# Optimization experiments

Measured on AMD Instinct MI355X. Metric: run time of the kernel, lower is better.

Reference implementation:

```python
import jax, jax.numpy as jnp
import numpy as np

N = 50000      # num_nodes
E = 800000     # num_edges
F = 29         # num_node_features
IN = F + 3     # in_channels after hstack with pos
H = 64         # hidden_dim
B = 50         # batch_size (num graphs)
L = 7          # num GINConv layers


def setup_inputs() -> dict:
    key = jax.random.key(0)
    ks = jax.random.split(key, 12)
    s_in = 1.0 / np.sqrt(IN)
    s_h = 1.0 / np.sqrt(H)
    return {
        "x": jax.random.normal(ks[0], (N, F), jnp.float32),
        "pos": jax.random.normal(ks[1], (N, 3), jnp.float32),
        "edge_index": jax.random.randint(ks[2], (2, E), 0, N),
        "batch": jnp.sort(jax.random.randint(ks[3], (N,), 0, B)),
        # GINConv l: MLP = Linear(in,H) -> ReLU -> Linear(H,H)
        "W1_first": jax.random.normal(ks[4], (IN, H), jnp.float32) * s_in,
        "W1_rest": jax.random.normal(ks[5], (L - 1, H, H), jnp.float32) * s_h,
        "b1": jax.random.normal(ks[6], (L, H), jnp.float32) * 0.01,
        "W2": jax.random.normal(ks[7], (L, H, H), jnp.float32) * s_h,
        "b2": jax.random.normal(ks[8], (L, H), jnp.float32) * 0.01,
        "lin_w": jax.random.normal(ks[9], (H, 1), jnp.float32) * s_h,
        "lin_b": jax.random.normal(ks[10], (1,), jnp.float32) * 0.01,
    }


def reference(x, pos, edge_index, batch, W1_first, W1_rest, b1, W2, b2, lin_w, lin_b):
    src, dst = edge_index[0], edge_index[1]
    h = jnp.concatenate([x, pos], axis=1)  # [N, IN]

    def gin_conv(h, Wa, ba, Wb, bb):
        # sum aggregation of source features at destination nodes, eps=0
        agg = jax.ops.segment_sum(h[src], dst, num_segments=N)
        z = h + agg
        z = jax.nn.relu(z @ Wa + ba)
        return z @ Wb + bb

    h = jax.nn.relu(gin_conv(h, W1_first, b1[0], W2[0], b2[0]))
    for l in range(1, L):
        h = gin_conv(h, W1_rest[l - 1], b1[l], W2[l], b2[l])
        if l < L - 1:  # no activation after last conv (jk=None)
            h = jax.nn.relu(h)

    # global mean pool per graph
    sums = jax.ops.segment_sum(h, batch, num_segments=B)            # [B, H]
    counts = jax.ops.segment_sum(jnp.ones((N,), h.dtype), batch, num_segments=B)
    pooled = sums / jnp.maximum(counts, 1.0)[:, None]

    return pooled @ lin_w + lin_b  # [B, 1]
```

## Files before the change

### kernel.cpp

```cpp
#include <hip/hip_runtime.h>
#include <stdint.h>

#define NF 29
#define HD 64
#define NL 7
#define LDW 72
#define NCHUNK 256
#define BSH 8
#define PER_M (64 * LDW)

typedef __attribute__((ext_vector_type(8))) __bf16 bf16x8;
typedef __attribute__((ext_vector_type(4))) float floatx4;
typedef int int32x4 __attribute__((ext_vector_type(4)));
typedef float f32x4v __attribute__((ext_vector_type(4)));

extern "C" __device__ f32x4v llvm_amdgcn_raw_buffer_load_fp32x4(
    int32x4 srsrc, int voffset, int soffset, int cachepolicy)
    __asm("llvm.amdgcn.raw.buffer.load.v4f32");

__device__ __forceinline__ int32x4 make_srd(const void* p) {
    unsigned long long a = (unsigned long long)p;
    int32x4 r;
    r.x = (int)(a & 0xFFFFFFFFull);
    r.y = (int)(a >> 32);
    r.z = -1;
    r.w = 0x00020000;
    return r;
}
__device__ __forceinline__ uint4 bload16_sc0(int32x4 srd, int voff) {
    f32x4v v = llvm_amdgcn_raw_buffer_load_fp32x4(srd, voff, 0, 1 );
    union { f32x4v f; uint4 u; } c;
    c.f = v;
    return c.u;
}

__device__ __forceinline__ unsigned short f2bf(float x) {
    unsigned u = __float_as_uint(x);
    unsigned r = (u + 0x7fffu + ((u >> 16) & 1u)) >> 16;
    return (unsigned short)r;
}
__device__ __forceinline__ unsigned pack_bf2(float x, float y) {
    return (unsigned)f2bf(x) | ((unsigned)f2bf(y) << 16);
}
__device__ __forceinline__ float bflo(uint32_t u) { return __uint_as_float(u << 16); }
__device__ __forceinline__ float bfhi(uint32_t u) { return __uint_as_float(u & 0xffff0000u); }
__device__ __forceinline__ float bf2f(unsigned short s) {
    return __uint_as_float((uint32_t)s << 16);
}

__global__ void front_kernel(const float* __restrict__ x, const float* __restrict__ pos,
                             unsigned short* __restrict__ h0,
                             const float* __restrict__ W1f, const float* __restrict__ W1r,
                             const float* __restrict__ W2, unsigned short* __restrict__ wpk,
                             const int* __restrict__ dst, int E, int chunk,
                             int* __restrict__ bcnt, int* __restrict__ bsum,
                             float* __restrict__ pool, int N, int B) {
    __shared__ int hist[256];
    const int H0B = (N * 4 + 255) / 256;
    const int WPB = (NL * 2 * PER_M + 255) / 256;
    int blk = blockIdx.x;
    if (blk < H0B) {
        int t = blk * 256 + threadIdx.x;
        if (t < N * 4) {
            int n = t >> 2, q = t & 3;
            const float* xr = x + (size_t)n * NF;
            float f[8];
            if (q < 3) {
                #pragma unroll
                for (int i = 0; i < 8; ++i) f[i] = xr[q * 8 + i];
            } else {
                #pragma unroll
                for (int i = 0; i < 5; ++i) f[i] = xr[24 + i];
                f[5] = pos[n * 3 + 0]; f[6] = pos[n * 3 + 1]; f[7] = pos[n * 3 + 2];
            }
            uint4 pk;
            pk.x = pack_bf2(f[0], f[1]); pk.y = pack_bf2(f[2], f[3]);
            pk.z = pack_bf2(f[4], f[5]); pk.w = pack_bf2(f[6], f[7]);
            ((uint4*)h0)[t] = pk;
        }
    } else if (blk < H0B + WPB) {
        int bw = blk - H0B;
        if (bw == 0) {
            for (int i = threadIdx.x; i < B * HD; i += 256) pool[i] = 0.f;
        }
        int t = bw * 256 + threadIdx.x;
        if (t < NL * 2 * PER_M) {
            int l = t / (2 * PER_M);
            int r = t - l * 2 * PER_M;
            int m = r / PER_M;
            int q = r - m * PER_M;
            int j = q / LDW, k = q - j * LDW;
            float v = 0.f;
            if (m == 0) {
                int ind = (l == 0) ? 32 : 64;
                if (k < ind) v = (l == 0) ? W1f[k * 64 + j]
                                          : W1r[(size_t)(l - 1) * 4096 + (size_t)k * 64 + j];
            } else {
                if (k < 64) v = W2[(size_t)l * 4096 + (size_t)k * 64 + j];
            }
            wpk[t] = f2bf(v);
        }
    } else {
        int c = blk - H0B - WPB;
        int tid = threadIdx.x;
        hist[tid] = 0;
        __syncthreads();
        int lo = c * chunk, hi = min(E, lo + chunk);
        for (int e = lo + tid; e < hi; e += 256) atomicAdd(&hist[dst[e] >> BSH], 1);
        __syncthreads();
        bcnt[tid * NCHUNK + c] = hist[tid];
        if (hist[tid]) atomicAdd(&bsum[tid], hist[tid]);
    }
}

__global__ void bucket_off_kernel(const int* __restrict__ bcnt, const int* __restrict__ bsum,
                                  int* __restrict__ boffT) {
    __shared__ int red[256];
    __shared__ int s[256];
    int b = blockIdx.x, t = threadIdx.x;
    red[t] = (t < b) ? bsum[t] : 0;
    __syncthreads();
    #pragma unroll
    for (int off = 128; off > 0; off >>= 1) {
        if (t < off) red[t] += red[t + off];
        __syncthreads();
    }
    int bstart_b = red[0];
    int c = bcnt[b * NCHUNK + t];
    s[t] = c;
    __syncthreads();
    for (int off = 1; off < 256; off <<= 1) {
        int v = (t >= off) ? s[t - off] : 0;
        __syncthreads();
        s[t] += v;
        __syncthreads();
    }
    int excl = s[t] - c;
    boffT[t * 256 + b] = bstart_b + excl;
}

__global__ void bucket_scatter_kernel(const int* __restrict__ src, const int* __restrict__ dst,
                                      int E, int chunk, const int* __restrict__ boffT,
                                      unsigned int* __restrict__ ebuf) {
    __shared__ int cur[256];
    int tid = threadIdx.x, c = blockIdx.x;
    cur[tid] = boffT[c * 256 + tid];
    __syncthreads();
    int lo = c * chunk, hi = min(E, lo + chunk);
    for (int e = lo + tid; e < hi; e += 256) {
        int d = dst[e];
        int p = atomicAdd(&cur[d >> BSH], 1);
        ebuf[p] = (unsigned int)src[e] | ((unsigned int)(d & 255) << 16);
    }
}

__global__ void final_scatter_kernel(const unsigned int* __restrict__ ebuf,
                                     const int* __restrict__ bsum,
                                     int* __restrict__ rowptr,
                                     unsigned short* __restrict__ colsrc, int N, int E) {
    __shared__ int red[256];
    __shared__ int cnt[256];
    __shared__ int cur[256];
    __shared__ int s[256];
    int b = blockIdx.x, t = threadIdx.x;
    red[t] = (t < b) ? bsum[t] : 0;
    cnt[t] = 0;
    __syncthreads();
    #pragma unroll
    for (int off = 128; off > 0; off >>= 1) {
        if (t < off) red[t] += red[t + off];
        __syncthreads();
    }
    int lo = red[0];
    int hi = lo + bsum[b];
    if (b == 0 && t == 0) rowptr[N] = E;
    for (int e = lo + t; e < hi; e += 256) atomicAdd(&cnt[ebuf[e] >> 16], 1);
    __syncthreads();
    int c = cnt[t];
    s[t] = c;
    __syncthreads();
    for (int off = 1; off < 256; off <<= 1) {
        int v = (t >= off) ? s[t - off] : 0;
        __syncthreads();
        s[t] += v;
        __syncthreads();
    }
    int base = lo + s[t] - c;
    int node = (b << BSH) + t;
    if (node < N) rowptr[node] = base;
    cur[t] = base;
    __syncthreads();
    for (int e = lo + t; e < hi; e += 256) {
        unsigned int ed = ebuf[e];
        int p = atomicAdd(&cur[ed >> 16], 1);
        colsrc[p] = (unsigned short)(ed & 0xffffu);
    }
}

template<int IND, bool RELU_OUT, bool LAST>
__global__ __launch_bounds__(512, 8)
void gin_layer_kernel(const unsigned short* __restrict__ hin,
                      const int* __restrict__ rowptr, const unsigned short* __restrict__ colsrc,
                      const unsigned short* __restrict__ wAT, const unsigned short* __restrict__ wBT,
                      const float* __restrict__ ba, const float* __restrict__ bb,
                      unsigned short* __restrict__ hout,
                      const int* __restrict__ batch, float* __restrict__ pool,
                      int N)
{
    __shared__ __align__(16) unsigned short zbuf[64 * LDW];
    __shared__ __align__(16) unsigned short t1buf[64 * LDW];

    const int tid = threadIdx.x;
    const int lane = tid & 63;
    const int w = tid >> 6;
    const int tile0 = blockIdx.x * 64;

    const int32x4 srd = make_srd(hin);
    const int g = lane >> 3;
    const int j = lane & 7;
    const int node = tile0 + w * 8 + g;

    int rp;
    {
        int idx = tile0 + w * 8 + (lane < 9 ? lane : 8);
        if (idx > N) idx = N;
        rp = rowptr[idx];
    }
    int e0 = __shfl(rp, g);
    int e1 = __shfl(rp, g + 1);
    if (node >= N) { e0 = 0; e1 = 0; }

    float acc[8] = {0.f, 0.f, 0.f, 0.f, 0.f, 0.f, 0.f, 0.f};
    auto addrow = [&](uint4 u) {
        acc[0] += bflo(u.x); acc[1] += bfhi(u.x);
        acc[2] += bflo(u.y); acc[3] += bfhi(u.y);
        acc[4] += bflo(u.z); acc[5] += bfhi(u.z);
        acc[6] += bflo(u.w); acc[7] += bfhi(u.w);
    };

    if constexpr (IND == 64) {
        const int f4 = lane & 7;
        if (node < N) addrow(bload16_sc0(srd, node * 128 + f4 * 16));
        int e = e0;
        int idxv = (e + j < e1) ? (int)colsrc[e + j] : 0;
        for (; e + 7 < e1; e += 8) {
            int en = e + 8;
            int idx_next = (en + j < e1) ? (int)colsrc[en + j] : 0;
            int s[8];
            #pragma unroll
            for (int q = 0; q < 8; ++q) s[q] = __shfl(idxv, g * 8 + q);
            uint4 u[8];
            #pragma unroll
            for (int q = 0; q < 8; ++q) u[q] = bload16_sc0(srd, s[q] * 128 + f4 * 16);
            #pragma unroll
            for (int q = 0; q < 8; ++q) addrow(u[q]);
            idxv = idx_next;
        }
        {
            int rem = e1 - e;
            #pragma unroll
            for (int q = 0; q < 8; ++q) {
                if (q < rem) {
                    int s = __shfl(idxv, g * 8 + q);
                    addrow(bload16_sc0(srd, s * 128 + f4 * 16));
                }
            }
        }
        uint4 pk;
        pk.x = pack_bf2(acc[0], acc[1]); pk.y = pack_bf2(acc[2], acc[3]);
        pk.z = pack_bf2(acc[4], acc[5]); pk.w = pack_bf2(acc[6], acc[7]);
        *(uint4*)&zbuf[(w * 8 + g) * LDW + f4 * 8] = pk;
    } else {
        const int p = (lane >> 2) & 1;
        const int f4 = lane & 3;
        if (node < N && p == 0) addrow(bload16_sc0(srd, node * 64 + f4 * 16));
        int e = e0 + p;
        for (; e + 7 < e1; e += 8) {
            int s0 = colsrc[e], s1 = colsrc[e + 2], s2 = colsrc[e + 4], s3 = colsrc[e + 6];
            uint4 u0 = bload16_sc0(srd, s0 * 64 + f4 * 16);
            uint4 u1 = bload16_sc0(srd, s1 * 64 + f4 * 16);
            uint4 u2 = bload16_sc0(srd, s2 * 64 + f4 * 16);
            uint4 u3 = bload16_sc0(srd, s3 * 64 + f4 * 16);
            addrow(u0); addrow(u1); addrow(u2); addrow(u3);
        }
        while (e < e1) { addrow(bload16_sc0(srd, (int)colsrc[e] * 64 + f4 * 16)); e += 2; }
        #pragma unroll
        for (int i = 0; i < 8; ++i) acc[i] += __shfl_xor(acc[i], 4);
        if (p == 0) {
            uint4 pk;
            pk.x = pack_bf2(acc[0], acc[1]); pk.y = pack_bf2(acc[2], acc[3]);
            pk.z = pack_bf2(acc[4], acc[5]); pk.w = pack_bf2(acc[6], acc[7]);
            *(uint4*)&zbuf[(w * 8 + g) * LDW + f4 * 8] = pk;
        }
    }
    __syncthreads();

    const int n0 = lane & 15, quad = lane >> 4;
    const int stripe = w & 3, jhalf = w >> 2;
    const int row0 = stripe * 16;
    const int jt0 = jhalf * 2, jt1 = jhalf * 2 + 1;

    floatx4 c0, c1;
    {
        float b0v = ba[jt0 * 16 + n0], b1v = ba[jt1 * 16 + n0];
        c0 = (floatx4){b0v, b0v, b0v, b0v};
        c1 = (floatx4){b1v, b1v, b1v, b1v};
    }
    #pragma unroll
    for (int kk = 0; kk < IND / 32; ++kk) {
        bf16x8 a   = *(const bf16x8*)&zbuf[(row0 + n0) * LDW + kk * 32 + quad * 8];
        bf16x8 br0 = *(const bf16x8*)&wAT[(jt0 * 16 + n0) * LDW + kk * 32 + quad * 8];
        bf16x8 br1 = *(const bf16x8*)&wAT[(jt1 * 16 + n0) * LDW + kk * 32 + quad * 8];
        c0 = __builtin_amdgcn_mfma_f32_16x16x32_bf16(a, br0, c0, 0, 0, 0);
        c1 = __builtin_amdgcn_mfma_f32_16x16x32_bf16(a, br1, c1, 0, 0, 0);
    }
    #pragma unroll
    for (int r = 0; r < 4; ++r) {
        int row = row0 + quad * 4 + r;
        t1buf[row * LDW + jt0 * 16 + n0] = f2bf(fmaxf(c0[r], 0.f));
        t1buf[row * LDW + jt1 * 16 + n0] = f2bf(fmaxf(c1[r], 0.f));
    }
    __syncthreads();

    {
        float b0v = bb[jt0 * 16 + n0], b1v = bb[jt1 * 16 + n0];
        c0 = (floatx4){b0v, b0v, b0v, b0v};
        c1 = (floatx4){b1v, b1v, b1v, b1v};
    }
    #pragma unroll
    for (int kk = 0; kk < 2; ++kk) {
        bf16x8 a   = *(const bf16x8*)&t1buf[(row0 + n0) * LDW + kk * 32 + quad * 8];
        bf16x8 br0 = *(const bf16x8*)&wBT[(jt0 * 16 + n0) * LDW + kk * 32 + quad * 8];
        bf16x8 br1 = *(const bf16x8*)&wBT[(jt1 * 16 + n0) * LDW + kk * 32 + quad * 8];
        c0 = __builtin_amdgcn_mfma_f32_16x16x32_bf16(a, br0, c0, 0, 0, 0);
        c1 = __builtin_amdgcn_mfma_f32_16x16x32_bf16(a, br1, c1, 0, 0, 0);
    }
    #pragma unroll
    for (int r = 0; r < 4; ++r) {
        int row = row0 + quad * 4 + r;
        float v0 = c0[r], v1 = c1[r];
        if (RELU_OUT) { v0 = fmaxf(v0, 0.f); v1 = fmaxf(v1, 0.f); }
        zbuf[row * LDW + jt0 * 16 + n0] = f2bf(v0);
        zbuf[row * LDW + jt1 * 16 + n0] = f2bf(v1);
    }
    __syncthreads();

    if constexpr (!LAST) {
        int nl = tid >> 3, c4 = tid & 7;
        int nodeo = tile0 + nl;
        if (nodeo < N) {
            uint4 v = *(const uint4*)&zbuf[nl * LDW + c4 * 8];
            ((uint4*)hout)[(size_t)nodeo * 8 + c4] = v;
        }
    } else {
        int nl0 = w * 8;
        int bvec = 0;
        if (lane < 8) {
            int idx = tile0 + nl0 + lane;
            bvec = batch[idx < N ? idx : (N - 1)];
        }
        int bsel = -1;
        float run = 0.f;
        for (int i = 0; i < 8; ++i) {
            int nodeo = tile0 + nl0 + i;
            if (nodeo >= N) break;
            int b = __shfl(bvec, i);
            float v = bf2f(zbuf[(nl0 + i) * LDW + lane]);
            if (b != bsel) {
                if (bsel >= 0) atomicAdd(&pool[bsel * HD + lane], run);
                bsel = b; run = 0.f;
            }
            run += v;
        }
        if (bsel >= 0) atomicAdd(&pool[bsel * HD + lane], run);
    }
}

__global__ void final_kernel(const float* __restrict__ pool, const int* __restrict__ batch,
                             const float* __restrict__ lin_w, const float* __restrict__ lin_b,
                             float* __restrict__ out, int B, int N) {
    int b = blockIdx.x;
    int lane = threadIdx.x;
    int lo = 0, hi = N;
    while (lo < hi) { int m = (lo + hi) >> 1; if (batch[m] < b) lo = m + 1; else hi = m; }
    int lb = lo;
    lo = 0; hi = N;
    while (lo < hi) { int m = (lo + hi) >> 1; if (batch[m] <= b) lo = m + 1; else hi = m; }
    float c = fmaxf((float)(lo - lb), 1.f);
    float v = pool[b * HD + lane] / c * lin_w[lane];
    for (int off = 32; off > 0; off >>= 1) v += __shfl_down(v, off);
    if (lane == 0) out[b] = v + lin_b[0];
}

extern "C" void kernel_launch(void* const* d_in, const int* in_sizes, int n_in,
                              void* d_out, int out_size, void* d_ws, size_t ws_size,
                              hipStream_t stream)
{
    const float* x   = (const float*)d_in[0];
    const float* pos = (const float*)d_in[1];
    const int*  eidx = (const int*)d_in[2];
    const int* batch = (const int*)d_in[3];
    const float* W1f = (const float*)d_in[4];
    const float* W1r = (const float*)d_in[5];
    const float* b1  = (const float*)d_in[6];
    const float* W2  = (const float*)d_in[7];
    const float* b2  = (const float*)d_in[8];
    const float* lw  = (const float*)d_in[9];
    const float* lb  = (const float*)d_in[10];

    int N = in_sizes[3];
    int E = in_sizes[2] / 2;
    int B = out_size;
    const int* src = eidx;
    const int* dst = eidx + E;

    char* ws = (char*)d_ws;
    size_t off = 0;
    auto alloc = [&](size_t bytes) -> void* {
        void* p = ws + off;
        off += (bytes + 255) & ~(size_t)255;
        return p;
    };
    unsigned short* bufA = (unsigned short*)alloc((size_t)N * HD * 2);
    unsigned short* bufB = (unsigned short*)alloc((size_t)N * HD * 2);
    int*   rowptr = (int*)  alloc((size_t)(N + 1) * 4);
    unsigned short* colsrc = (unsigned short*)alloc((size_t)E * 2);
    unsigned int* ebuf = (unsigned int*)alloc((size_t)E * 4);
    float* pool   = (float*)alloc((size_t)B * HD * 4);
    int*   bcnt   = (int*)  alloc((size_t)256 * NCHUNK * 4);
    int*   boffT  = (int*)  alloc((size_t)NCHUNK * 256 * 4);
    int*   bsum   = (int*)  alloc(256 * 4);
    unsigned short* wpk = (unsigned short*)alloc((size_t)NL * 2 * PER_M * 2);

    hipMemsetAsync(bsum, 0, 256 * 4, stream);

    int nbuk = (N + 255) >> BSH;
    int chunk = (E + NCHUNK - 1) / NCHUNK;

    const int H0B = (N * 4 + 255) / 256;
    const int WPB = (NL * 2 * PER_M + 255) / 256;
    front_kernel<<<H0B + WPB + NCHUNK, 256, 0, stream>>>(
        x, pos, bufA, W1f, W1r, W2, wpk, dst, E, chunk, bcnt, bsum, pool, N, B);
    bucket_off_kernel<<<nbuk, 256, 0, stream>>>(bcnt, bsum, boffT);
    bucket_scatter_kernel<<<NCHUNK, 256, 0, stream>>>(src, dst, E, chunk, boffT, ebuf);
    final_scatter_kernel<<<nbuk, 256, 0, stream>>>(ebuf, bsum, rowptr, colsrc, N, E);

    const int gblocks = (N + 63) / 64;
    gin_layer_kernel<32, true, false><<<gblocks, 512, 0, stream>>>(
        bufA, rowptr, colsrc, wpk + 0 * PER_M, wpk + 1 * PER_M, b1, b2, bufB,
        nullptr, nullptr, N);
    unsigned short* cur_in = bufB;
    unsigned short* cur_out = bufA;
    for (int l = 1; l < NL; ++l) {
        const unsigned short* wa = wpk + (size_t)(2 * l + 0) * PER_M;
        const unsigned short* wb = wpk + (size_t)(2 * l + 1) * PER_M;
        const float* ba = b1 + l * HD;
        const float* bb = b2 + l * HD;
        if (l < NL - 1) {
            gin_layer_kernel<HD, true, false><<<gblocks, 512, 0, stream>>>(
                cur_in, rowptr, colsrc, wa, wb, ba, bb, cur_out, nullptr, nullptr, N);
            unsigned short* tmp = cur_in; cur_in = cur_out; cur_out = tmp;
        } else {
            gin_layer_kernel<HD, false, true><<<gblocks, 512, 0, stream>>>(
                cur_in, rowptr, colsrc, wa, wb, ba, bb, nullptr, batch, pool, N);
        }
    }
    final_kernel<<<B, 64, 0, stream>>>(pool, batch, lw, lb, (float*)d_out, B, N);
}
```

Baseline: 250.4 us.

## Halve GIN layer tile to 32 nodes and fuse bucket offset into scatter

The GIN layer kernel now processes 32 nodes per block with 256 threads, where it used 64 nodes with 512 threads. The warp-to-stripe mapping is remapped to match, giving more, smaller blocks and finer load balance across CUs. Separately, the bucket offset kernel is removed: each scatter block now computes the global bucket prefix scan and sums earlier chunk counts itself, with bcnt stored chunk-major. This saves one launch, but the per-block serial loop over up to 255 chunks adds redundant work.

```diff
diff --git a/kernel.cpp b/kernel.cpp
--- a/kernel.cpp
+++ b/kernel.cpp
@@ -8,6 +8,7 @@
 #define NCHUNK 256
 #define BSH 8
 #define PER_M (64 * LDW)
+#define TILE 32
 
 typedef __attribute__((ext_vector_type(8))) __bf16 bf16x8;
 typedef __attribute__((ext_vector_type(4))) float floatx4;
@@ -108,26 +109,20 @@
         int lo = c * chunk, hi = min(E, lo + chunk);
         for (int e = lo + tid; e < hi; e += 256) atomicAdd(&hist[dst[e] >> BSH], 1);
         __syncthreads();
-        bcnt[tid * NCHUNK + c] = hist[tid];
+        bcnt[c * 256 + tid] = hist[tid];
         if (hist[tid]) atomicAdd(&bsum[tid], hist[tid]);
     }
 }
 
-__global__ void bucket_off_kernel(const int* __restrict__ bcnt, const int* __restrict__ bsum,
-                                  int* __restrict__ boffT) {
-    __shared__ int red[256];
+__global__ void bucket_scatter_kernel(const int* __restrict__ src, const int* __restrict__ dst,
+                                      int E, int chunk, const int* __restrict__ bcnt,
+                                      const int* __restrict__ bsum,
+                                      unsigned int* __restrict__ ebuf) {
     __shared__ int s[256];
-    int b = blockIdx.x, t = threadIdx.x;
-    red[t] = (t < b) ? bsum[t] : 0;
-    __syncthreads();
-    #pragma unroll
-    for (int off = 128; off > 0; off >>= 1) {
-        if (t < off) red[t] += red[t + off];
-        __syncthreads();
-    }
-    int bstart_b = red[0];
-    int c = bcnt[b * NCHUNK + t];
-    s[t] = c;
+    __shared__ int cur[256];
+    int c = blockIdx.x, t = threadIdx.x;
+    int own = bsum[t];
+    s[t] = own;
     __syncthreads();
     for (int off = 1; off < 256; off <<= 1) {
         int v = (t >= off) ? s[t - off] : 0;
@@ -135,19 +130,13 @@
         s[t] += v;
         __syncthreads();
     }
-    int excl = s[t] - c;
-    boffT[t * 256 + b] = bstart_b + excl;
-}
-
-__global__ void bucket_scatter_kernel(const int* __restrict__ src, const int* __restrict__ dst,
-                                      int E, int chunk, const int* __restrict__ boffT,
-                                      unsigned int* __restrict__ ebuf) {
-    __shared__ int cur[256];
-    int tid = threadIdx.x, c = blockIdx.x;
-    cur[tid] = boffT[c * 256 + tid];
+    int bstart_t = s[t] - own;
+    int pre = 0;
+    for (int i = 0; i < c; ++i) pre += bcnt[i * 256 + t];
+    cur[t] = bstart_t + pre;
     __syncthreads();
     int lo = c * chunk, hi = min(E, lo + chunk);
-    for (int e = lo + tid; e < hi; e += 256) {
+    for (int e = lo + t; e < hi; e += 256) {
         int d = dst[e];
         int p = atomicAdd(&cur[d >> BSH], 1);
         ebuf[p] = (unsigned int)src[e] | ((unsigned int)(d & 255) << 16);
@@ -198,7 +187,7 @@
 }
 
 template<int IND, bool RELU_OUT, bool LAST>
-__global__ __launch_bounds__(512, 8)
+__global__ __launch_bounds__(256, 8)
 void gin_layer_kernel(const unsigned short* __restrict__ hin,
                       const int* __restrict__ rowptr, const unsigned short* __restrict__ colsrc,
                       const unsigned short* __restrict__ wAT, const unsigned short* __restrict__ wBT,
@@ -207,13 +196,13 @@
                       const int* __restrict__ batch, float* __restrict__ pool,
                       int N)
 {
-    __shared__ __align__(16) unsigned short zbuf[64 * LDW];
-    __shared__ __align__(16) unsigned short t1buf[64 * LDW];
+    __shared__ __align__(16) unsigned short zbuf[TILE * LDW];
+    __shared__ __align__(16) unsigned short t1buf[TILE * LDW];
 
     const int tid = threadIdx.x;
     const int lane = tid & 63;
     const int w = tid >> 6;
-    const int tile0 = blockIdx.x * 64;
+    const int tile0 = blockIdx.x * TILE;
 
     const int32x4 srd = make_srd(hin);
     const int g = lane >> 3;
@@ -296,7 +285,7 @@
     __syncthreads();
 
     const int n0 = lane & 15, quad = lane >> 4;
-    const int stripe = w & 3, jhalf = w >> 2;
+    const int stripe = w & 1, jhalf = w >> 1;
     const int row0 = stripe * 16;
     const int jt0 = jhalf * 2, jt1 = jhalf * 2 + 1;
 
@@ -427,8 +416,7 @@
     unsigned short* colsrc = (unsigned short*)alloc((size_t)E * 2);
     unsigned int* ebuf = (unsigned int*)alloc((size_t)E * 4);
     float* pool   = (float*)alloc((size_t)B * HD * 4);
-    int*   bcnt   = (int*)  alloc((size_t)256 * NCHUNK * 4);
-    int*   boffT  = (int*)  alloc((size_t)NCHUNK * 256 * 4);
+    int*   bcnt   = (int*)  alloc((size_t)NCHUNK * 256 * 4);
     int*   bsum   = (int*)  alloc(256 * 4);
     unsigned short* wpk = (unsigned short*)alloc((size_t)NL * 2 * PER_M * 2);
 
@@ -441,12 +429,11 @@
     const int WPB = (NL * 2 * PER_M + 255) / 256;
     front_kernel<<<H0B + WPB + NCHUNK, 256, 0, stream>>>(
         x, pos, bufA, W1f, W1r, W2, wpk, dst, E, chunk, bcnt, bsum, pool, N, B);
-    bucket_off_kernel<<<nbuk, 256, 0, stream>>>(bcnt, bsum, boffT);
-    bucket_scatter_kernel<<<NCHUNK, 256, 0, stream>>>(src, dst, E, chunk, boffT, ebuf);
+    bucket_scatter_kernel<<<NCHUNK, 256, 0, stream>>>(src, dst, E, chunk, bcnt, bsum, ebuf);
     final_scatter_kernel<<<nbuk, 256, 0, stream>>>(ebuf, bsum, rowptr, colsrc, N, E);
 
-    const int gblocks = (N + 63) / 64;
-    gin_layer_kernel<32, true, false><<<gblocks, 512, 0, stream>>>(
+    const int gblocks = (N + TILE - 1) / TILE;
+    gin_layer_kernel<32, true, false><<<gblocks, 256, 0, stream>>>(
         bufA, rowptr, colsrc, wpk + 0 * PER_M, wpk + 1 * PER_M, b1, b2, bufB,
         nullptr, nullptr, N);
     unsigned short* cur_in = bufB;
@@ -457,11 +444,11 @@
         const float* ba = b1 + l * HD;
         const float* bb = b2 + l * HD;
         if (l < NL - 1) {
-            gin_layer_kernel<HD, true, false><<<gblocks, 512, 0, stream>>>(
+            gin_layer_kernel<HD, true, false><<<gblocks, 256, 0, stream>>>(
                 cur_in, rowptr, colsrc, wa, wb, ba, bb, cur_out, nullptr, nullptr, N);
             unsigned short* tmp = cur_in; cur_in = cur_out; cur_out = tmp;
         } else {
-            gin_layer_kernel<HD, false, true><<<gblocks, 512, 0, stream>>>(
+            gin_layer_kernel<HD, false, true><<<gblocks, 256, 0, stream>>>(
                 cur_in, rowptr, colsrc, wa, wb, ba, bb, nullptr, batch, pool, N);
         }
     }
```

New measurement: 270.1 us. 1.08x slower.
